# Kernel optimization log

Hardware: AMD Instinct MI355X
Metric: run time of the kernel (lower is better)

Reference implementation:

```python
import jax, jax.numpy as jnp
import numpy as np

B, S, D, H, F = 2, 1024, 2048, 16, 8192
DH = D // H
MAX_ALPHA = 0.2
CN_SCALE = D / (D - 1)  # CenterNorm scale factor dim/(dim-1)


def setup_inputs() -> dict:
    key = jax.random.key(0)
    ks = jax.random.split(key, 8)
    s = 0.02
    f32 = jnp.float32
    return {
        "x": jax.random.normal(ks[0], (B, S, D), f32),
        "ln1_g": jnp.ones((D,), f32), "ln1_b": jnp.zeros((D,), f32),
        "wq": jax.random.normal(ks[1], (D, D), f32) * s, "bq": jnp.zeros((D,), f32),
        "wk": jax.random.normal(ks[2], (D, D), f32) * s, "bk": jnp.zeros((D,), f32),
        "wv": jax.random.normal(ks[3], (D, D), f32) * s, "bv": jnp.zeros((D,), f32),
        "wo": jax.random.normal(ks[4], (D, D), f32) * s, "bo": jnp.zeros((D,), f32),
        "tau": jnp.ones((H,), f32),   # learnable per-head temperature, init_tau=1.0
        "nu": jnp.ones((H,), f32),    # learnable per-head output scale, init_nu=1.0
        "alpha1": jnp.full((D,), 0.1, f32),  # per-channel residual weight, init 0.1
        "ln2_g": jnp.ones((D,), f32), "ln2_b": jnp.zeros((D,), f32),
        "w1": jax.random.normal(ks[5], (F, D), f32) * s, "b1": jnp.zeros((F,), f32),
        "w2": jax.random.normal(ks[6], (D, F), f32) * s, "b2": jnp.zeros((D,), f32),
        "alpha2": jnp.full((D,), 0.1, f32),
    }


def _center_norm(x, g, b):
    # CenterNorm: subtract mean only (no variance), scale by dim/(dim-1)
    mu = jnp.mean(x, axis=-1, keepdims=True)
    return g * (CN_SCALE * (x - mu)) + b


def _l2norm(t):
    return t / (jnp.linalg.norm(t, axis=-1, keepdims=True) + 1e-6)


def _cosine_attn(x, wq, bq, wk, bk, wv, bv, wo, bo, tau, nu):
    # project and split heads -> [B,H,S,DH]
    def proj(w, b):
        return (jnp.einsum('bsd,ed->bse', x, w) + b).reshape(B, S, H, DH).transpose(0, 2, 1, 3)
    q, k, v = proj(wq, bq), proj(wk, bk), proj(wv, bv)
    qn, kn = _l2norm(q), _l2norm(k)  # cosine similarity attention
    scores = jnp.einsum('bhqd,bhkd->bhqk', qn, kn) * tau[None, :, None, None]
    causal = jnp.tril(jnp.ones((S, S), bool))
    scores = jnp.where(causal[None, None], scores, -jnp.inf)
    p = jax.nn.softmax(scores, axis=-1)
    o = jnp.einsum('bhqk,bhkd->bhqd', p, v) * nu[None, :, None, None]
    o = o.transpose(0, 2, 1, 3).reshape(B, S, D)
    return jnp.einsum('bsd,ed->bse', o, wo) + bo


def _ffn(x, w1, b1, w2, b2):
    h = jax.nn.gelu(jnp.einsum('bsd,fd->bsf', x, w1) + b1)
    return jnp.einsum('bsf,df->bsd', h, w2) + b2


def reference(x, ln1_g, ln1_b, wq, bq, wk, bk, wv, bv, wo, bo, tau, nu,
              alpha1, ln2_g, ln2_b, w1, b1, w2, b2, alpha2):
    a = _center_norm(x, ln1_g, ln1_b)
    a1 = jnp.clip(alpha1, -MAX_ALPHA, MAX_ALPHA)
    x1 = a + a1 * _cosine_attn(a, wq, bq, wk, bk, wv, bv, wo, bo, tau, nu)
    m = _center_norm(x1, ln2_g, ln2_b)
    a2 = jnp.clip(alpha2, -MAX_ALPHA, MAX_ALPHA)
    return m + a2 * _ffn(m, w1, b1, w2, b2)
```

## Files before the change

### kernel.cpp

```cpp
#include <hip/hip_runtime.h>
#include <hip/hip_bf16.h>
#include <stdint.h>

#define B_ 2
#define S_ 1024
#define D_ 2048
#define H_ 16
#define F_ 8192
#define DH_ 128
#define M_ 2048

typedef unsigned short u16;
typedef __attribute__((ext_vector_type(8))) short short8;
typedef __attribute__((ext_vector_type(4))) float f32x4;
typedef __attribute__((ext_vector_type(2))) float f32x2;

__device__ __forceinline__ u16 f2bf(float f) {
  union { float f; uint32_t u; } c; c.f = f;
  uint32_t r = c.u + 0x7FFFu + ((c.u >> 16) & 1u);
  return (u16)(r >> 16);
}

__device__ __forceinline__ float bf2f(u16 v) {
  union { uint32_t u; float f; } c; c.u = ((uint32_t)v) << 16;
  return c.f;
}

__device__ __forceinline__ void gload16(const void* g, void* l) {
  __builtin_amdgcn_global_load_lds((const __attribute__((address_space(1))) void*)g,
                                   (__attribute__((address_space(3))) void*)l, 16, 0, 0);
}

__device__ __forceinline__ float clipa(float a) {
  return fminf(0.2f, fmaxf(-0.2f, a));
}

__device__ __forceinline__ float gelu_f(float x) {
  float z = 0.7978845608028654f * (x + 0.044715f * x * x * x);
  z = fminf(10.f, fmaxf(-10.f, z));
  float e = __expf(2.f * z);
  return 0.5f * x * (1.f + (e - 1.f) / (e + 1.f));
}

__global__ __launch_bounds__(256) void k_cn1_cvt(const float* __restrict__ x,
                                                 const float* __restrict__ g,
                                                 const float* __restrict__ bb,
                                                 float* __restrict__ of,
                                                 u16* __restrict__ ob,
                                                 const float* __restrict__ wq,
                                                 const float* __restrict__ wk,
                                                 const float* __restrict__ wv,
                                                 const float* __restrict__ wo,
                                                 u16* __restrict__ dstW) {
  if (blockIdx.x >= 2048) {
    const int gi = (blockIdx.x - 2048) * 256 + threadIdx.x;
    const int r = gi >> 19;
    const float* s = r == 0 ? wq : (r == 1 ? wk : (r == 2 ? wv : wo));
    const int off = gi & 524287;
    f32x4 a = *(const f32x4*)(s + (size_t)off * 8);
    f32x4 b = *(const f32x4*)(s + (size_t)off * 8 + 4);
    short8 o;
    o[0] = (short)f2bf(a[0]); o[1] = (short)f2bf(a[1]);
    o[2] = (short)f2bf(a[2]); o[3] = (short)f2bf(a[3]);
    o[4] = (short)f2bf(b[0]); o[5] = (short)f2bf(b[1]);
    o[6] = (short)f2bf(b[2]); o[7] = (short)f2bf(b[3]);
    *(short8*)(dstW + (size_t)gi * 8) = o;
    return;
  }
  const int row = blockIdx.x;
  const int t = threadIdx.x;
  const float* xr = x + (size_t)row * D_;
  f32x4 v0 = *(const f32x4*)(xr + t * 8);
  f32x4 v1 = *(const f32x4*)(xr + t * 8 + 4);
  float s = v0[0] + v0[1] + v0[2] + v0[3] + v1[0] + v1[1] + v1[2] + v1[3];
#pragma unroll
  for (int off = 1; off < 64; off <<= 1) s += __shfl_xor(s, off);
  __shared__ float red[4];
  if ((t & 63) == 0) red[t >> 6] = s;
  __syncthreads();
  const float mu = (red[0] + red[1] + red[2] + red[3]) * (1.0f / D_);
  const float CNS = (float)D_ / (float)(D_ - 1);
  f32x4 g0 = *(const f32x4*)(g + t * 8);
  f32x4 g1 = *(const f32x4*)(g + t * 8 + 4);
  f32x4 b0 = *(const f32x4*)(bb + t * 8);
  f32x4 b1 = *(const f32x4*)(bb + t * 8 + 4);
  f32x4 y0, y1;
  short8 yb;
#pragma unroll
  for (int i = 0; i < 4; i++) {
    y0[i] = g0[i] * (CNS * (v0[i] - mu)) + b0[i];
    y1[i] = g1[i] * (CNS * (v1[i] - mu)) + b1[i];
  }
#pragma unroll
  for (int i = 0; i < 4; i++) { yb[i] = (short)f2bf(y0[i]); yb[4 + i] = (short)f2bf(y1[i]); }
  float* orow = of + (size_t)row * D_;
  *(f32x4*)(orow + t * 8) = y0;
  *(f32x4*)(orow + t * 8 + 4) = y1;
  *(short8*)(ob + (size_t)row * D_ + t * 8) = yb;
}

__global__ __launch_bounds__(256) void k_centernorm(const float* __restrict__ x,
                                                    const float* __restrict__ g,
                                                    const float* __restrict__ bb,
                                                    float* __restrict__ of,
                                                    u16* __restrict__ ob) {
  const int row = blockIdx.x;
  const int t = threadIdx.x;
  const float* xr = x + (size_t)row * D_;
  f32x4 v0 = *(const f32x4*)(xr + t * 8);
  f32x4 v1 = *(const f32x4*)(xr + t * 8 + 4);
  float s = v0[0] + v0[1] + v0[2] + v0[3] + v1[0] + v1[1] + v1[2] + v1[3];
#pragma unroll
  for (int off = 1; off < 64; off <<= 1) s += __shfl_xor(s, off);
  __shared__ float red[4];
  if ((t & 63) == 0) red[t >> 6] = s;
  __syncthreads();
  const float mu = (red[0] + red[1] + red[2] + red[3]) * (1.0f / D_);
  const float CNS = (float)D_ / (float)(D_ - 1);
  f32x4 g0 = *(const f32x4*)(g + t * 8);
  f32x4 g1 = *(const f32x4*)(g + t * 8 + 4);
  f32x4 b0 = *(const f32x4*)(bb + t * 8);
  f32x4 b1 = *(const f32x4*)(bb + t * 8 + 4);
  f32x4 y0, y1;
  short8 yb;
#pragma unroll
  for (int i = 0; i < 4; i++) {
    y0[i] = g0[i] * (CNS * (v0[i] - mu)) + b0[i];
    y1[i] = g1[i] * (CNS * (v1[i] - mu)) + b1[i];
  }
#pragma unroll
  for (int i = 0; i < 4; i++) { yb[i] = (short)f2bf(y0[i]); yb[4 + i] = (short)f2bf(y1[i]); }
  float* orow = of + (size_t)row * D_;
  *(f32x4*)(orow + t * 8) = y0;
  *(f32x4*)(orow + t * 8 + 4) = y1;
  *(short8*)(ob + (size_t)row * D_ + t * 8) = yb;
}

template <int EPI>
__device__ __forceinline__ void gemm256_core(const u16* __restrict__ A,
                                             const u16* __restrict__ Bt,
                                             const float* __restrict__ bias,
                                             u16* __restrict__ outb,
                                             int N, int K, int kbase, int nk,
                                             int m0, int n0,
                                             const float* __restrict__ tau,
                                             u16* __restrict__ qkv, int z) {
  __shared__ char lds[2][65536];
  const int t = threadIdx.x;
  const int l = t & 63, w = t >> 6;
  const int wr = w >> 2, wc = w & 3;
  const int l15 = l & 15, lhi = l >> 4;
  const int sw = (l15 & 7) << 4;
  const int ab0 = l15 * 128 + ((lhi * 16) ^ sw);
  const int ab1 = l15 * 128 + ((64 + lhi * 16) ^ sw);

  auto stage = [&](int kt, int h) {
#pragma unroll
    for (int rj = 0; rj < 4; rj++) {
      const int region = rj >> 1, j = rj & 1;
      const int pl = h * 16384 + j * 8192 + t * 16;
      const int row = pl >> 7;
      const int scol = (pl & 127) ^ ((row & 7) << 4);
      const int grow = (region ? n0 : m0) + row;
      const char* src = (const char*)(region ? Bt : A) +
                        (size_t)grow * (size_t)(K * 2) +
                        (size_t)((kbase + kt * 64) * 2 + scol);
      gload16(src, &lds[kt & 1][region * 32768 + pl]);
    }
  };

  f32x4 acc[8][4] = {};

  stage(0, 0); stage(0, 1); stage(1, 0);
  asm volatile("s_waitcnt vmcnt(4)" ::: "memory");
  __builtin_amdgcn_s_barrier();
  __builtin_amdgcn_sched_barrier(0);

  for (int kt = 0; kt < nk; ++kt) {
    const char* base = &lds[kt & 1][0];
    const char* pA0 = base + wr * 4096 + ab0;
    const char* pA1 = base + wr * 4096 + ab1;
    const char* pB0 = base + 32768 + wc * 8192 + ab0;
    const char* pB1 = base + 32768 + wc * 8192 + ab1;
    short8 bf[4][2];
#pragma unroll
    for (int ni = 0; ni < 4; ni++) {
      bf[ni][0] = *(const short8*)(pB0 + ni * 2048);
      bf[ni][1] = *(const short8*)(pB1 + ni * 2048);
    }
#pragma unroll
    for (int q = 0; q < 4; q++) {
      short8 aq[2][2];
#pragma unroll
      for (int mi = 0; mi < 2; mi++) {
        aq[mi][0] = *(const short8*)(pA0 + q * 8192 + mi * 2048);
        aq[mi][1] = *(const short8*)(pA1 + q * 8192 + mi * 2048);
      }
      if (q == 1 && kt + 1 < nk) stage(kt + 1, 1);
      if (q == 3 && kt + 2 < nk) stage(kt + 2, 0);
      __builtin_amdgcn_s_setprio(1);
#pragma unroll
      for (int ks = 0; ks < 2; ks++)
#pragma unroll
        for (int mi = 0; mi < 2; mi++)
#pragma unroll
          for (int ni = 0; ni < 4; ni++)
            acc[q * 2 + mi][ni] = __builtin_amdgcn_mfma_f32_16x16x32_bf16(
                aq[mi][ks], bf[ni][ks], acc[q * 2 + mi][ni], 0, 0, 0);
      __builtin_amdgcn_s_setprio(0);
      if (q == 1) __builtin_amdgcn_s_barrier();
    }
    if (kt + 1 < nk) {
      if (kt + 2 < nk) { asm volatile("s_waitcnt vmcnt(4)" ::: "memory"); }
      else             { asm volatile("s_waitcnt vmcnt(0)" ::: "memory"); }
      __builtin_amdgcn_s_barrier();
      __builtin_amdgcn_sched_barrier(0);
    }
  }

  if constexpr (EPI == 4) {
    __shared__ float part[4][256];
#pragma unroll
    for (int ni = 0; ni < 4; ni++) {
      const float bc = bias[n0 + wc * 64 + ni * 16 + l15];
#pragma unroll
      for (int ai = 0; ai < 8; ai++)
#pragma unroll
        for (int j = 0; j < 4; j++) acc[ai][ni][j] += bc;
    }
    if (z < 2) {
      float p[8][4];
#pragma unroll
      for (int ai = 0; ai < 8; ai++)
#pragma unroll
        for (int j = 0; j < 4; j++) {
          p[ai][j] = acc[ai][0][j] * acc[ai][0][j] + acc[ai][1][j] * acc[ai][1][j] +
                     acc[ai][2][j] * acc[ai][2][j] + acc[ai][3][j] * acc[ai][3][j];
#pragma unroll
          for (int off = 1; off < 16; off <<= 1) p[ai][j] += __shfl_xor(p[ai][j], off);
        }
      if (l15 == 0) {
#pragma unroll
        for (int ai = 0; ai < 8; ai++)
#pragma unroll
          for (int j = 0; j < 4; j++) {
            const int rb = (ai >> 1) * 64 + wr * 32 + (ai & 1) * 16 + lhi * 4 + j;
            part[wc][rb] = p[ai][j];
          }
      }
    }
    __syncthreads();
    const int hl = wc >> 1;
    const int hglob = (n0 >> 7) + hl;
    const float tauh = (z == 0) ? tau[hglob] : 1.f;
    char* yt = (char*)&lds[0][0] + w * 16384;
#pragma unroll
    for (int ai = 0; ai < 8; ai++) {
#pragma unroll
      for (int j = 0; j < 4; j++) {
        float sc = 1.f;
        if (z < 2) {
          const int rb = (ai >> 1) * 64 + wr * 32 + (ai & 1) * 16 + lhi * 4 + j;
          const float ssq = part[2 * hl][rb] + part[2 * hl + 1][rb];
          sc = tauh / (sqrtf(ssq) + 1e-6f);
        }
        const int rl = (ai >> 1) * 32 + (ai & 1) * 16 + lhi * 4 + j;
        const int swz = (rl & 7) << 4;
#pragma unroll
        for (int ni = 0; ni < 4; ni++) {
          const int cbyte = (ni * 16 + l15) * 2;
          *(u16*)(yt + rl * 128 + (cbyte ^ swz)) = f2bf(acc[ai][ni][j] * sc);
        }
      }
    }
    __syncthreads();
#pragma unroll
    for (int pass = 0; pass < 16; pass++) {
      const int rl = pass * 8 + (l >> 3);
      const int cb = (l & 7) * 16;
      const short8 v = *(const short8*)(yt + rl * 128 + (cb ^ ((rl & 7) << 4)));
      const int m = m0 + ((rl >> 5) << 6) + wr * 32 + (rl & 31);
      const int bb2 = m >> 10, s = m & 1023;
      const int d = (wc & 1) * 64 + (cb >> 1);
      *(short8*)(qkv + (((size_t)(bb2 * H_ + hglob)) * S_ + s) * DH_ + d) = v;
    }
    return;
  }

#pragma unroll
  for (int ni = 0; ni < 4; ni++) {
    const int col = n0 + wc * 64 + ni * 16 + l15;
    const float bcol = (EPI == 3) ? 0.f : bias[col];
#pragma unroll
    for (int ai = 0; ai < 8; ai++) {
      const int row = m0 + (ai >> 1) * 64 + wr * 32 + (ai & 1) * 16 + lhi * 4;
#pragma unroll
      for (int j = 0; j < 4; j++) {
        const float v = acc[ai][ni][j] + bcol;
        const size_t idx = (size_t)(row + j) * N + col;
        if (EPI == 2) outb[idx] = f2bf(gelu_f(v));
        else outb[idx] = f2bf(v);
      }
    }
  }
}

__global__ __launch_bounds__(512, 2) void k_qkv256(const u16* A, const u16* W,
                                                   const float* b0, const float* b1,
                                                   const float* b2, const float* tau,
                                                   u16* qn, u16* kn, u16* vn) {
  const int z = blockIdx.z;
  const u16* Bt = W + (size_t)z * 4194304;
  const float* bias = z == 0 ? b0 : (z == 1 ? b1 : b2);
  u16* dst = z == 0 ? qn : (z == 1 ? kn : vn);
  gemm256_core<4>(A, Bt, bias, nullptr, D_, D_, 0, 32,
                  blockIdx.y * 256, blockIdx.x * 256, tau, dst, z);
}

__global__ __launch_bounds__(512, 2) void k_ffn1_256(const u16* A, const u16* Bt,
                                                     const float* bias, u16* outb) {
  gemm256_core<2>(A, Bt, bias, outb, F_, D_, 0, 32,
                  blockIdx.y * 256, blockIdx.x * 256, nullptr, nullptr, 0);
}

__global__ __launch_bounds__(512, 2) void k_ffn2_256(const u16* A, const u16* Bt, u16* P) {
  gemm256_core<3>(A, Bt, nullptr, P + (size_t)blockIdx.z * M_ * D_, D_, F_,
                  blockIdx.z * 2048, 32, blockIdx.y * 256, blockIdx.x * 256,
                  nullptr, nullptr, 0);
}

__global__ __launch_bounds__(256, 2) void k_oproj(const u16* __restrict__ A,
                                                  const u16* __restrict__ Bt,
                                                  const float* __restrict__ bias,
                                                  const float* __restrict__ res,
                                                  const float* __restrict__ alpha,
                                                  float* __restrict__ outf) {
  const int N = D_, K = D_, nk = 32;
  const int m0 = blockIdx.y * 128, n0 = blockIdx.x * 128;
  __shared__ char lds[2][32768];
  const int t = threadIdx.x;
  const int l = t & 63, w = t >> 6;
  const int wr = w >> 1, wc = w & 1;
  const int l15 = l & 15, lhi = l >> 4;
  const int sw = (l15 & 7) << 4;
  const int ab0 = l15 * 128 + ((lhi * 16) ^ sw);
  const int ab1 = l15 * 128 + ((64 + lhi * 16) ^ sw);

  auto stage = [&](int kt, int h) {
#pragma unroll
    for (int rj = 0; rj < 4; rj++) {
      const int region = rj >> 1, j = rj & 1;
      const int pl = h * 8192 + j * 4096 + t * 16;
      const int row = pl >> 7;
      const int scol = (pl & 127) ^ ((row & 7) << 4);
      const int grow = (region ? n0 : m0) + row;
      const char* src = (const char*)(region ? Bt : A) +
                        (size_t)grow * (size_t)(K * 2) + (size_t)(kt * 128 + scol);
      gload16(src, &lds[kt & 1][region * 16384 + pl]);
    }
  };

  f32x4 acc[4][4] = {};
  stage(0, 0); stage(0, 1); stage(1, 0);
  asm volatile("s_waitcnt vmcnt(4)" ::: "memory");
  __builtin_amdgcn_s_barrier();
  __builtin_amdgcn_sched_barrier(0);

  for (int kt = 0; kt < nk; ++kt) {
    const char* base = &lds[kt & 1][0];
    const char* pB0 = base + 16384 + wc * 8192 + ab0;
    const char* pB1 = base + 16384 + wc * 8192 + ab1;
    short8 bf[4][2];
#pragma unroll
    for (int ni = 0; ni < 4; ni++) {
      bf[ni][0] = *(const short8*)(pB0 + ni * 2048);
      bf[ni][1] = *(const short8*)(pB1 + ni * 2048);
    }
#pragma unroll
    for (int q = 0; q < 2; q++) {
      short8 aq[2][2];
#pragma unroll
      for (int mi = 0; mi < 2; mi++) {
        aq[mi][0] = *(const short8*)(base + q * 8192 + wr * 4096 + mi * 2048 + ab0);
        aq[mi][1] = *(const short8*)(base + q * 8192 + wr * 4096 + mi * 2048 + ab1);
      }
      if (q == 0 && kt + 1 < nk) stage(kt + 1, 1);
      if (q == 1 && kt + 2 < nk) stage(kt + 2, 0);
      __builtin_amdgcn_s_setprio(1);
#pragma unroll
      for (int ks = 0; ks < 2; ks++)
#pragma unroll
        for (int mi = 0; mi < 2; mi++)
#pragma unroll
          for (int ni = 0; ni < 4; ni++)
            acc[q * 2 + mi][ni] = __builtin_amdgcn_mfma_f32_16x16x32_bf16(
                aq[mi][ks], bf[ni][ks], acc[q * 2 + mi][ni], 0, 0, 0);
      __builtin_amdgcn_s_setprio(0);
      if (q == 0) __builtin_amdgcn_s_barrier();
    }
    if (kt + 1 < nk) {
      if (kt + 2 < nk) { asm volatile("s_waitcnt vmcnt(4)" ::: "memory"); }
      else             { asm volatile("s_waitcnt vmcnt(0)" ::: "memory"); }
      __builtin_amdgcn_s_barrier();
      __builtin_amdgcn_sched_barrier(0);
    }
  }

#pragma unroll
  for (int ni = 0; ni < 4; ni++) {
    const int col = n0 + wc * 64 + ni * 16 + l15;
    const float bcol = bias[col];
    const float alc = clipa(alpha[col]);
#pragma unroll
    for (int ai = 0; ai < 4; ai++) {
      const int row = m0 + (ai >> 1) * 64 + wr * 32 + (ai & 1) * 16 + lhi * 4;
#pragma unroll
      for (int j = 0; j < 4; j++) {
        const size_t idx = (size_t)(row + j) * N + col;
        outf[idx] = res[idx] + alc * (acc[ai][ni][j] + bcol);
      }
    }
  }
}

__global__ __launch_bounds__(256) void k_ffn2_combine(const u16* __restrict__ P,
                                                      const float* __restrict__ bias,
                                                      const float* __restrict__ res,
                                                      const float* __restrict__ alpha,
                                                      float* __restrict__ out) {
  const int i = blockIdx.x * 256 + threadIdx.x;
  const size_t base = (size_t)i * 8;
  const int col = (int)(base & (D_ - 1));
  const size_t PS = (size_t)M_ * D_;
  float s[8] = {};
#pragma unroll
  for (int p = 0; p < 4; p++) {
    short8 v = *(const short8*)(P + p * PS + base);
#pragma unroll
    for (int j = 0; j < 8; j++) s[j] += bf2f((u16)v[j]);
  }
  f32x4 b0 = *(const f32x4*)(bias + col);
  f32x4 b1 = *(const f32x4*)(bias + col + 4);
  f32x4 a0 = *(const f32x4*)(alpha + col);
  f32x4 a1 = *(const f32x4*)(alpha + col + 4);
  f32x4 r0 = *(const f32x4*)(res + base);
  f32x4 r1 = *(const f32x4*)(res + base + 4);
  f32x4 o0, o1;
#pragma unroll
  for (int j = 0; j < 4; j++) {
    o0[j] = r0[j] + clipa(a0[j]) * (s[j] + b0[j]);
    o1[j] = r1[j] + clipa(a1[j]) * (s[4 + j] + b1[j]);
  }
  *(f32x4*)(out + base) = o0;
  *(f32x4*)(out + base + 4) = o1;
}

__global__ __launch_bounds__(256) void k_attn(const u16* __restrict__ qn,
                                              const u16* __restrict__ kn,
                                              const u16* __restrict__ vn,
                                              const float* __restrict__ nu,
                                              u16* __restrict__ o,
                                              const float* __restrict__ w1,
                                              const float* __restrict__ w2,
                                              u16* __restrict__ W12) {
  __shared__ u16 Ks[64 * 128];
  __shared__ u16 Vt[128 * 64];
  __shared__ u16 Pl[4][16][72];
  if (blockIdx.x >= 512) {
    const int gi = (blockIdx.x - 512) * 256 + threadIdx.x;
    const float* s = (gi < 2097152) ? w1 : w2;
    const int off = (gi < 2097152) ? gi : gi - 2097152;
    f32x4 a = *(const f32x4*)(s + (size_t)off * 8);
    f32x4 b = *(const f32x4*)(s + (size_t)off * 8 + 4);
    short8 ov;
    ov[0] = (short)f2bf(a[0]); ov[1] = (short)f2bf(a[1]);
    ov[2] = (short)f2bf(a[2]); ov[3] = (short)f2bf(a[3]);
    ov[4] = (short)f2bf(b[0]); ov[5] = (short)f2bf(b[1]);
    ov[6] = (short)f2bf(b[2]); ov[7] = (short)f2bf(b[3]);
    *(short8*)(W12 + (size_t)gi * 8) = ov;
    return;
  }
  const int t = threadIdx.x;
  const int l = t & 63, w = t >> 6;
  const int l15 = l & 15, lhi = l >> 4;
  const int qt = blockIdx.x & 15;
  const int bh = blockIdx.x >> 4;
  const int h = bh & (H_ - 1);
  const int b = bh >> 4;
  const size_t hoff = (size_t)bh * S_ * DH_;
  const u16* Qh = qn + hoff;
  const u16* Kh = kn + hoff;
  const u16* Vh = vn + hoff;
  const int q0 = qt * 64;
  const int r0 = q0 + w * 16;
  short8 qf[4];
#pragma unroll
  for (int kk = 0; kk < 4; kk++)
    qf[kk] = *(const short8*)(Qh + (size_t)(r0 + l15) * DH_ + kk * 32 + lhi * 8);
  float mrow[4], lrow[4];
  f32x4 oacc[8] = {};
#pragma unroll
  for (int j = 0; j < 4; j++) { mrow[j] = -1e30f; lrow[j] = 0.f; }

  for (int kv0 = 0; kv0 < q0 + 64; kv0 += 64) {
#pragma unroll
    for (int i = 0; i < 4; i++) {
      const int p = i * 4096 + t * 16;
      const int row = p >> 8;
      const int colb = p & 255;
      const int scolb = colb ^ ((row & 7) << 4);
      gload16((const char*)(Kh + (size_t)(kv0 + row) * DH_) + scolb, (char*)Ks + p);
    }
#pragma unroll
    for (int i = 0; i < 4; i++) {
      const int c0 = w * 8 + i * 32;
      const int r = l;
      short8 vv = *(const short8*)(Vh + (size_t)(kv0 + r) * DH_ + c0);
#pragma unroll
      for (int j = 0; j < 8; j++) {
        const int ba = ((c0 + j) * 128 + r * 2) ^ (((c0 + j) & 7) << 4);
        *(u16*)((char*)Vt + ba) = (u16)vv[j];
      }
    }
    __syncthreads();
    f32x4 st[4] = {};
#pragma unroll
    for (int ks = 0; ks < 4; ks++) {
#pragma unroll
      for (int ct = 0; ct < 4; ct++) {
        const int n = ct * 16 + l15;
        const int ka = (ks * 32 + lhi * 8) * 2;
        short8 kf = *(const short8*)((const char*)Ks + n * 256 + (ka ^ ((n & 7) << 4)));
        st[ct] = __builtin_amdgcn_mfma_f32_16x16x32_bf16(qf[ks], kf, st[ct], 0, 0, 0);
      }
    }
    float pm[4] = {-1e30f, -1e30f, -1e30f, -1e30f};
#pragma unroll
    for (int ct = 0; ct < 4; ct++) {
      const int col = kv0 + ct * 16 + l15;
#pragma unroll
      for (int j = 0; j < 4; j++) {
        const int row = r0 + lhi * 4 + j;
        float s = st[ct][j];
        s = (col <= row) ? s : -1e30f;
        st[ct][j] = s;
        pm[j] = fmaxf(pm[j], s);
      }
    }
#pragma unroll
    for (int j = 0; j < 4; j++) {
#pragma unroll
      for (int off = 1; off < 16; off <<= 1) pm[j] = fmaxf(pm[j], __shfl_xor(pm[j], off));
    }
    float scl[4], psum[4];
#pragma unroll
    for (int j = 0; j < 4; j++) {
      const float nm = fmaxf(mrow[j], pm[j]);
      scl[j] = __expf(mrow[j] - nm);
      mrow[j] = nm;
      psum[j] = 0.f;
    }
#pragma unroll
    for (int ct = 0; ct < 4; ct++) {
#pragma unroll
      for (int j = 0; j < 4; j++) {
        const float p = __expf(st[ct][j] - mrow[j]);
        psum[j] += p;
        Pl[w][lhi * 4 + j][ct * 16 + l15] = f2bf(p);
      }
    }
#pragma unroll
    for (int j = 0; j < 4; j++) {
#pragma unroll
      for (int off = 1; off < 16; off <<= 1) psum[j] += __shfl_xor(psum[j], off);
      lrow[j] = lrow[j] * scl[j] + psum[j];
    }
#pragma unroll
    for (int nt = 0; nt < 8; nt++) {
#pragma unroll
      for (int j = 0; j < 4; j++) oacc[nt][j] *= scl[j];
    }
#pragma unroll
    for (int ks2 = 0; ks2 < 2; ks2++) {
      short8 pa = *(const short8*)((const char*)&Pl[w][0][0] + l15 * 144 + ks2 * 64 + lhi * 16);
#pragma unroll
      for (int nt = 0; nt < 8; nt++) {
        const int n = nt * 16 + l15;
        const int ba = (n * 128 + (ks2 * 32 + lhi * 8) * 2) ^ ((n & 7) << 4);
        short8 vf = *(const short8*)((const char*)Vt + ba);
        oacc[nt] = __builtin_amdgcn_mfma_f32_16x16x32_bf16(pa, vf, oacc[nt], 0, 0, 0);
      }
    }
    __syncthreads();
  }
  const float num = nu[h];
  float rs[4];
#pragma unroll
  for (int j = 0; j < 4; j++) rs[j] = num / lrow[j];
#pragma unroll
  for (int nt = 0; nt < 8; nt++) {
    const int col = h * DH_ + nt * 16 + l15;
#pragma unroll
    for (int j = 0; j < 4; j++) {
      const int row = r0 + lhi * 4 + j;
      o[((size_t)b * S_ + row) * D_ + col] = f2bf(oacc[nt][j] * rs[j]);
    }
  }
}

extern "C" void kernel_launch(void* const* d_in, const int* in_sizes, int n_in,
                              void* d_out, int out_size, void* d_ws, size_t ws_size,
                              hipStream_t stream) {
  const float* x    = (const float*)d_in[0];
  const float* ln1g = (const float*)d_in[1];
  const float* ln1b = (const float*)d_in[2];
  const float* wq   = (const float*)d_in[3];
  const float* bq   = (const float*)d_in[4];
  const float* wk   = (const float*)d_in[5];
  const float* bk   = (const float*)d_in[6];
  const float* wv   = (const float*)d_in[7];
  const float* bv   = (const float*)d_in[8];
  const float* wo   = (const float*)d_in[9];
  const float* bo   = (const float*)d_in[10];
  const float* tau  = (const float*)d_in[11];
  const float* nu   = (const float*)d_in[12];
  const float* al1  = (const float*)d_in[13];
  const float* ln2g = (const float*)d_in[14];
  const float* ln2b = (const float*)d_in[15];
  const float* w1   = (const float*)d_in[16];
  const float* b1   = (const float*)d_in[17];
  const float* w2   = (const float*)d_in[18];
  const float* b2   = (const float*)d_in[19];
  const float* al2  = (const float*)d_in[20];

  char* ws = (char*)d_ws;
  u16* WQ = (u16*)(ws + 0);
  u16* WO = (u16*)(ws + 25165824);
  u16* W1B = (u16*)(ws + 33554432);
  float* AF = (float*)(ws + 100663296);
  u16*   AB = (u16*)(ws + 117440512);
  u16*   OB = (u16*)(ws + 125829120);
  u16*   MB = (u16*)(ws + 134217728);
  float* X1 = (float*)(ws + 142606336);
  float* MF2 = (float*)(ws + 159383552);
  u16* QN = (u16*)(ws + 176160768);
  u16* KN = (u16*)(ws + 184549376);
  u16* VN = (u16*)(ws + 192937984);
  u16*   HB = (u16*)(ws + 176160768);
  u16*   P4 = (u16*)(ws + 0);
  u16* W2B = (u16*)(ws + 67108864);

  k_cn1_cvt<<<10240, 256, 0, stream>>>(x, ln1g, ln1b, AF, AB, wq, wk, wv, wo, WQ);

  k_qkv256<<<dim3(8, 8, 3), 512, 0, stream>>>(AB, WQ, bq, bk, bv, tau, QN, KN, VN);

  k_attn<<<16896, 256, 0, stream>>>(QN, KN, VN, nu, OB, w1, w2, W1B);

  k_oproj<<<dim3(16, 16), 256, 0, stream>>>(OB, WO, bo, AF, al1, X1);

  k_centernorm<<<M_, 256, 0, stream>>>(X1, ln2g, ln2b, MF2, MB);

  k_ffn1_256<<<dim3(32, 8), 512, 0, stream>>>(MB, W1B, b1, HB);

  k_ffn2_256<<<dim3(8, 8, 4), 512, 0, stream>>>(HB, W2B, P4);
  k_ffn2_combine<<<2048, 256, 0, stream>>>(P4, b2, MF2, al2, (float*)d_out);
}
```

Baseline: 369.9 us.

## Overlap fp32-to-bf16 weight conversion with GEMM main loops

Moves the conversion of wo and w1 to bf16 out of the attention kernel and the cn1 prologue and into the QKV GEMM's k-loop, and moves the w2 conversion into the FFN1 GEMM's k-loop. Each GEMM thread loads fp32 weights at the start of an iteration and stores the bf16 result mid-iteration. The goal is to hide this memory-bound conversion traffic behind MFMA work instead of running it as separate blocks. It adds global loads and stores, plus register pressure, inside the hot GEMM loops, which could disturb the tuned pipeline.

```diff
diff --git a/kernel.cpp b/kernel.cpp
--- a/kernel.cpp
+++ b/kernel.cpp
@@ -13,7 +13,6 @@
 typedef unsigned short u16;
 typedef __attribute__((ext_vector_type(8))) short short8;
 typedef __attribute__((ext_vector_type(4))) float f32x4;
-typedef __attribute__((ext_vector_type(2))) float f32x2;
 
 __device__ __forceinline__ u16 f2bf(float f) {
   union { float f; uint32_t u; } c; c.f = f;
@@ -50,12 +49,11 @@
                                                  const float* __restrict__ wq,
                                                  const float* __restrict__ wk,
                                                  const float* __restrict__ wv,
-                                                 const float* __restrict__ wo,
                                                  u16* __restrict__ dstW) {
   if (blockIdx.x >= 2048) {
     const int gi = (blockIdx.x - 2048) * 256 + threadIdx.x;
     const int r = gi >> 19;
-    const float* s = r == 0 ? wq : (r == 1 ? wk : (r == 2 ? wv : wo));
+    const float* s = r == 0 ? wq : (r == 1 ? wk : wv);
     const int off = gi & 524287;
     f32x4 a = *(const f32x4*)(s + (size_t)off * 8);
     f32x4 b = *(const f32x4*)(s + (size_t)off * 8 + 4);
@@ -136,7 +134,7 @@
   *(short8*)(ob + (size_t)row * D_ + t * 8) = yb;
 }
 
-template <int EPI>
+template <int EPI, bool CV>
 __device__ __forceinline__ void gemm256_core(const u16* __restrict__ A,
                                              const u16* __restrict__ Bt,
                                              const float* __restrict__ bias,
@@ -144,7 +142,13 @@
                                              int N, int K, int kbase, int nk,
                                              int m0, int n0,
                                              const float* __restrict__ tau,
-                                             u16* __restrict__ qkv, int z) {
+                                             u16* __restrict__ qkv, int z,
+                                             const float* __restrict__ cvA,
+                                             const float* __restrict__ cvB,
+                                             u16* __restrict__ cvdA,
+                                             u16* __restrict__ cvdB,
+                                             int cvsplit, int cvtotal,
+                                             int cvbf, int cvnb) {
   __shared__ char lds[2][65536];
   const int t = threadIdx.x;
   const int l = t & 63, w = t >> 6;
@@ -177,6 +181,24 @@
   __builtin_amdgcn_sched_barrier(0);
 
   for (int kt = 0; kt < nk; ++kt) {
+    f32x4 cv0, cv1;
+    u16* cdst = nullptr;
+    size_t coff = 0;
+    bool cdo = false;
+    if (CV) {
+      const int ui = (kt * cvnb + cvbf) * 512 + t;
+      if (ui < cvtotal) {
+        cdo = true;
+        int off = ui;
+        const float* csrc;
+        if (off < cvsplit) { csrc = cvA; cdst = cvdA; }
+        else { off -= cvsplit; csrc = cvB; cdst = cvdB; }
+        coff = (size_t)off * 8;
+        cv0 = *(const f32x4*)(csrc + coff);
+        cv1 = *(const f32x4*)(csrc + coff + 4);
+      }
+      __builtin_amdgcn_sched_barrier(0);
+    }
     const char* base = &lds[kt & 1][0];
     const char* pA0 = base + wr * 4096 + ab0;
     const char* pA1 = base + wr * 4096 + ab1;
@@ -197,7 +219,19 @@
         aq[mi][1] = *(const short8*)(pA1 + q * 8192 + mi * 2048);
       }
       if (q == 1 && kt + 1 < nk) stage(kt + 1, 1);
-      if (q == 3 && kt + 2 < nk) stage(kt + 2, 0);
+      if (q == 3) {
+        if (CV && cdo) {
+          short8 o;
+#pragma unroll
+          for (int e = 0; e < 4; e++) {
+            o[e] = (short)f2bf(cv0[e]);
+            o[4 + e] = (short)f2bf(cv1[e]);
+          }
+          *(short8*)(cdst + coff) = o;
+          __builtin_amdgcn_sched_barrier(0);
+        }
+        if (kt + 2 < nk) stage(kt + 2, 0);
+      }
       __builtin_amdgcn_s_setprio(1);
 #pragma unroll
       for (int ks = 0; ks < 2; ks++)
@@ -308,25 +342,33 @@
 __global__ __launch_bounds__(512, 2) void k_qkv256(const u16* A, const u16* W,
                                                    const float* b0, const float* b1,
                                                    const float* b2, const float* tau,
-                                                   u16* qn, u16* kn, u16* vn) {
+                                                   u16* qn, u16* kn, u16* vn,
+                                                   const float* wo, const float* w1,
+                                                   u16* WOB, u16* W1B) {
   const int z = blockIdx.z;
   const u16* Bt = W + (size_t)z * 4194304;
   const float* bias = z == 0 ? b0 : (z == 1 ? b1 : b2);
   u16* dst = z == 0 ? qn : (z == 1 ? kn : vn);
-  gemm256_core<4>(A, Bt, bias, nullptr, D_, D_, 0, 32,
-                  blockIdx.y * 256, blockIdx.x * 256, tau, dst, z);
+  const int bf = z * 64 + blockIdx.y * 8 + blockIdx.x;
+  gemm256_core<4, true>(A, Bt, bias, nullptr, D_, D_, 0, 32,
+                        blockIdx.y * 256, blockIdx.x * 256, tau, dst, z,
+                        wo, w1, WOB, W1B, 524288, 2621440, bf, 192);
 }
 
 __global__ __launch_bounds__(512, 2) void k_ffn1_256(const u16* A, const u16* Bt,
-                                                     const float* bias, u16* outb) {
-  gemm256_core<2>(A, Bt, bias, outb, F_, D_, 0, 32,
-                  blockIdx.y * 256, blockIdx.x * 256, nullptr, nullptr, 0);
+                                                     const float* bias, u16* outb,
+                                                     const float* w2, u16* W2B) {
+  const int bf = blockIdx.y * 32 + blockIdx.x;
+  gemm256_core<2, true>(A, Bt, bias, outb, F_, D_, 0, 32,
+                        blockIdx.y * 256, blockIdx.x * 256, nullptr, nullptr, 0,
+                        w2, nullptr, W2B, nullptr, 2097152, 2097152, bf, 256);
 }
 
 __global__ __launch_bounds__(512, 2) void k_ffn2_256(const u16* A, const u16* Bt, u16* P) {
-  gemm256_core<3>(A, Bt, nullptr, P + (size_t)blockIdx.z * M_ * D_, D_, F_,
-                  blockIdx.z * 2048, 32, blockIdx.y * 256, blockIdx.x * 256,
-                  nullptr, nullptr, 0);
+  gemm256_core<3, false>(A, Bt, nullptr, P + (size_t)blockIdx.z * M_ * D_, D_, F_,
+                         blockIdx.z * 2048, 32, blockIdx.y * 256, blockIdx.x * 256,
+                         nullptr, nullptr, 0,
+                         nullptr, nullptr, nullptr, nullptr, 0, 0, 0, 0);
 }
 
 __global__ __launch_bounds__(256, 2) void k_oproj(const u16* __restrict__ A,
@@ -459,32 +501,15 @@
                                               const u16* __restrict__ kn,
                                               const u16* __restrict__ vn,
                                               const float* __restrict__ nu,
-                                              u16* __restrict__ o,
-                                              const float* __restrict__ w1,
-                                              const float* __restrict__ w2,
-                                              u16* __restrict__ W12) {
+                                              u16* __restrict__ o) {
   __shared__ u16 Ks[64 * 128];
   __shared__ u16 Vt[128 * 64];
   __shared__ u16 Pl[4][16][72];
-  if (blockIdx.x >= 512) {
-    const int gi = (blockIdx.x - 512) * 256 + threadIdx.x;
-    const float* s = (gi < 2097152) ? w1 : w2;
-    const int off = (gi < 2097152) ? gi : gi - 2097152;
-    f32x4 a = *(const f32x4*)(s + (size_t)off * 8);
-    f32x4 b = *(const f32x4*)(s + (size_t)off * 8 + 4);
-    short8 ov;
-    ov[0] = (short)f2bf(a[0]); ov[1] = (short)f2bf(a[1]);
-    ov[2] = (short)f2bf(a[2]); ov[3] = (short)f2bf(a[3]);
-    ov[4] = (short)f2bf(b[0]); ov[5] = (short)f2bf(b[1]);
-    ov[6] = (short)f2bf(b[2]); ov[7] = (short)f2bf(b[3]);
-    *(short8*)(W12 + (size_t)gi * 8) = ov;
-    return;
-  }
   const int t = threadIdx.x;
   const int l = t & 63, w = t >> 6;
   const int l15 = l & 15, lhi = l >> 4;
-  const int qt = blockIdx.x & 15;
-  const int bh = blockIdx.x >> 4;
+  const int qt = blockIdx.x;
+  const int bh = blockIdx.y;
   const int h = bh & (H_ - 1);
   const int b = bh >> 4;
   const size_t hoff = (size_t)bh * S_ * DH_;
@@ -634,9 +659,10 @@
   const float* al2  = (const float*)d_in[20];
 
   char* ws = (char*)d_ws;
-  u16* WQ = (u16*)(ws + 0);
-  u16* WO = (u16*)(ws + 25165824);
+  u16* WQ  = (u16*)(ws + 0);
+  u16* WOB = (u16*)(ws + 25165824);
   u16* W1B = (u16*)(ws + 33554432);
+  u16* W2B = (u16*)(ws + 67108864);
   float* AF = (float*)(ws + 100663296);
   u16*   AB = (u16*)(ws + 117440512);
   u16*   OB = (u16*)(ws + 125829120);
@@ -648,19 +674,19 @@
   u16* VN = (u16*)(ws + 192937984);
   u16*   HB = (u16*)(ws + 176160768);
   u16*   P4 = (u16*)(ws + 0);
-  u16* W2B = (u16*)(ws + 67108864);
-
-  k_cn1_cvt<<<10240, 256, 0, stream>>>(x, ln1g, ln1b, AF, AB, wq, wk, wv, wo, WQ);
-
-  k_qkv256<<<dim3(8, 8, 3), 512, 0, stream>>>(AB, WQ, bq, bk, bv, tau, QN, KN, VN);
-
-  k_attn<<<16896, 256, 0, stream>>>(QN, KN, VN, nu, OB, w1, w2, W1B);
-
-  k_oproj<<<dim3(16, 16), 256, 0, stream>>>(OB, WO, bo, AF, al1, X1);
+
+  k_cn1_cvt<<<8192, 256, 0, stream>>>(x, ln1g, ln1b, AF, AB, wq, wk, wv, WQ);
+
+  k_qkv256<<<dim3(8, 8, 3), 512, 0, stream>>>(AB, WQ, bq, bk, bv, tau, QN, KN, VN,
+                                              wo, w1, WOB, W1B);
+
+  k_attn<<<dim3(S_ / 64, B_ * H_), 256, 0, stream>>>(QN, KN, VN, nu, OB);
+
+  k_oproj<<<dim3(16, 16), 256, 0, stream>>>(OB, WOB, bo, AF, al1, X1);
 
   k_centernorm<<<M_, 256, 0, stream>>>(X1, ln2g, ln2b, MF2, MB);
 
-  k_ffn1_256<<<dim3(32, 8), 512, 0, stream>>>(MB, W1B, b1, HB);
+  k_ffn1_256<<<dim3(32, 8), 512, 0, stream>>>(MB, W1B, b1, HB, w2, W2B);
 
   k_ffn2_256<<<dim3(8, 8, 4), 512, 0, stream>>>(HB, W2B, P4);
   k_ffn2_combine<<<2048, 256, 0, stream>>>(P4, b2, MF2, al2, (float*)d_out);
```

Measured after the change: 357.7 us. 3.3% less time.
